# Optimization experiments

Hardware: AMD Instinct MI355X
Metric: run time of the kernel (lower is better)

The kernel has to match this reference:

```python
import jax, jax.numpy as jnp
import numpy as np

N = 512      # num_neurons
D = 32       # delay_dim
T = 8192     # number of sequential timesteps
OMEGA = 10.0 # base_freq
ALPHA = 0.5
DT = 1e-3    # dt_global per tick
TWO_PI = float(2.0 * np.pi)


def setup_inputs() -> dict:
    key = jax.random.key(0)
    k = jax.random.split(key, 6)
    X_real = jax.random.normal(k[0], (T, D), jnp.float32)
    X_imag = jax.random.normal(k[1], (T, D), jnp.float32)
    target_wave = jax.random.normal(k[2], (T,), jnp.float32)
    # W initialized as torch.polar(rand*0.1, rand*2pi)
    mag = jax.random.uniform(k[3], (N, D), jnp.float32) * 0.1
    ang = jax.random.uniform(k[4], (N, D), jnp.float32) * TWO_PI
    W_real = mag * jnp.cos(ang)
    W_imag = mag * jnp.sin(ang)
    phi0 = jax.random.uniform(k[5], (N,), jnp.float32) * TWO_PI
    beta0 = jnp.linspace(0.005, 0.05, N, dtype=jnp.float32)
    return {"X_real": X_real, "X_imag": X_imag, "target_wave": target_wave,
            "W_real": W_real, "W_imag": W_imag, "phi0": phi0, "beta0": beta0}


def _run(X_real, X_imag, target_wave, W_real, W_imag, phi0, beta0):
    W0 = (W_real + 1j * W_imag).astype(jnp.complex64)   # [N, D]
    X = (X_real + 1j * X_imag).astype(jnp.complex64)    # [T, D]
    lt0 = jnp.zeros((N,), jnp.float32)                  # local_time
    err0 = jnp.float32(0.0)                             # err_smooth

    def step(carry, inp):
        W, phi, beta, lt, err = carry
        x, tgt = inp                                    # x: [D] complex, tgt: scalar
        gamma = jnp.exp(-ALPHA * beta)                  # time dilation Γ  [N]
        dt_local = gamma * DT                           # [N]
        lt = lt + dt_local
        Z = W @ x                                       # X_c @ W.T -> [N] complex
        theta = OMEGA * lt + phi                        # [N]
        gate = jax.nn.relu(jnp.cos(theta - jnp.angle(Z)))
        Y = jnp.abs(Z) * gate                           # [N] real
        out = jnp.sum(Y * jnp.cos(theta))               # Re(sum Y * exp(i theta))
        # thermodynamic error feedback (sequential dependency)
        raw_err = jnp.abs(tgt - out)
        err = 0.99 * err + 0.01 * raw_err
        rel_err = err / (jnp.abs(tgt) + 0.01)
        beta_target = 3.5 * jnp.exp(-5.0 * rel_err)
        tau = jnp.where(beta_target > beta, 0.5 / (gamma + 1e-6), 0.03)
        a_s = 1.0 - jnp.exp(-DT / tau)
        beta_new = jnp.clip(beta + a_s * (beta_target - beta), 0.005, 5.0)
        # Hebbian growth / viscous decay (growth.T and decay.T directly in [N,D])
        growth_t = 0.05 * Y[:, None] * x[None, :]                 # [N, D] complex
        decay_t = (beta_new * Y ** 2)[:, None].astype(jnp.complex64) * W
        W = W + (growth_t - decay_t) * dt_local[:, None].astype(jnp.complex64)
        # phase pull: imag(tgt * exp(-i theta)) = -tgt*sin(theta) for real tgt
        phi = jnp.mod(phi + (2.0 / N) * (-tgt * jnp.sin(theta)) * dt_local, TWO_PI)
        return (W, phi, beta_new, lt, err), (out, beta_new, gamma)

    _, (outs, betas, gammas) = jax.lax.scan(
        step, (W0, phi0, beta0, lt0, err0), (X, target_wave))
    return outs, betas, gammas


def reference(X_real, X_imag, target_wave, W_real, W_imag, phi0, beta0):
    return _run(X_real, X_imag, target_wave, W_real, W_imag, phi0, beta0)
```

## Files before the change

### kernel.cpp

```cpp
#include <hip/hip_runtime.h>

#define NN 512
#define DD 32
#define TT 8192

typedef float v4f __attribute__((ext_vector_type(4)));
typedef float v2f __attribute__((ext_vector_type(2)));
typedef __attribute__((address_space(3))) float lds_f;
typedef __attribute__((address_space(3))) void lds_v;
typedef const __attribute__((address_space(1))) void glb_v;

constexpr float F_OMEGA = 10.0f;
constexpr float F_DT = 1e-3f;
constexpr float F_TWO_PI = 6.28318530717958647692f;
constexpr float F_INV_TWO_PI = 0.15915494309189533577f;

__device__ __forceinline__ void barrier_lgkm() {
    asm volatile("s_waitcnt lgkmcnt(0)\n\ts_barrier" ::: "memory");
}

__device__ __forceinline__ void glds4(const float* g, lds_f* dst) {
    __builtin_amdgcn_global_load_lds((glb_v*)g, (lds_v*)dst, 4, 0, 0);
}

#define DSR128(dst, addr, off) \
    asm volatile("ds_read_b128 %0, %1 offset:" #off : "=v"(dst) : "v"(addr))
#define DSR32(dst, addr, off) \
    asm volatile("ds_read_b32 %0, %1 offset:" #off : "=v"(dst) : "v"(addr))

#define PK_MUL(d, a, b)  \
    asm("v_pk_mul_f32 %0, %1, %2" : "=v"(d) : "v"(a), "v"(b))
#define PK_FMA_ACC(d, a, b)  \
    asm("v_pk_fma_f32 %0, %1, %2, %0" : "+v"(d) : "v"(a), "v"(b))
#define PK_FMA_W(w, m, t)  \
    asm("v_pk_fma_f32 %0, %0, %1, %2" : "+v"(w) : "v"(m), "v"(t))

#define DPP_ADD(x, ctrl, rmask)                                                 \
    {                                                                           \
        int _t = __builtin_amdgcn_update_dpp(0, __float_as_int(x),              \
                                             (ctrl), (rmask), 0xf, true);       \
        (x) += __int_as_float(_t);                                              \
    }

__device__ __forceinline__ float wave_reduce_to_lane63(float x) {
    DPP_ADD(x, 0xB1, 0xf);
    DPP_ADD(x, 0x4E, 0xf);
    DPP_ADD(x, 0x141, 0xf);
    DPP_ADD(x, 0x140, 0xf);
    DPP_ADD(x, 0x142, 0xa);
    DPP_ADD(x, 0x143, 0xc);
    return x;
}

__global__ __launch_bounds__(512, 2) void deerskin(
    const float* __restrict__ Xr, const float* __restrict__ Xi,
    const float* __restrict__ Tg,
    const float* __restrict__ W0r, const float* __restrict__ W0i,
    const float* __restrict__ Phi0, const float* __restrict__ Beta0,
    float* __restrict__ outs, float* __restrict__ betas, float* __restrict__ gammas)
{
    __shared__ __align__(16) float xbuf[3][72];
    __shared__ __align__(16) float sP[16];

    const int n = threadIdx.x;
    const int lane = n & 63;
    const int wid = n >> 6;

    v2f wr2[16], wi2[16];
    {
        const v2f* wr0 = (const v2f*)(W0r + n * DD);
        const v2f* wi0 = (const v2f*)(W0i + n * DD);
#pragma unroll
        for (int k = 0; k < 16; ++k) { wr2[k] = wr0[k]; wi2[k] = wi0[k]; }
    }
    float phi = Phi0[n];
    float beta = Beta0[n];
    float lt = 0.0f;
    float err = 0.0f;

    const float* xsrc = ((lane < 32) ? Xr : Xi) + (lane & 31);

    lds_f* pcur = (lds_f*)&xbuf[0][0];
    lds_f* pnxt = (lds_f*)&xbuf[1][0];
    lds_f* pfut = (lds_f*)&xbuf[2][0];

    if (wid == 0) {
        glds4(xsrc, pcur);
        glds4(xsrc + DD, pnxt);
        if (lane == 0) {
            glds4(Tg, pcur + 64);
            glds4(Tg + 1, pnxt + 64);
        }
        asm volatile("s_waitcnt vmcnt(0)" ::: "memory");
    }
    barrier_lgkm();

    for (int t = 0; t < TT; ++t) {
        if (wid == 0) {
            int tf = t + 2; tf = (tf < TT) ? tf : (TT - 1);
            glds4(xsrc + (size_t)tf * DD, pfut);
            if (lane == 0) glds4(Tg + tf, pfut + 64);
        }

        const float gamma = __expf(-0.5f * beta);
        const float dtl = gamma * F_DT;
        lt += dtl;
        const float theta = fmaf(F_OMEGA, lt, phi);
        float rev = theta * F_INV_TWO_PI;
        rev -= floorf(rev);
        const float s = __builtin_amdgcn_sinf(rev);
        const float c = __builtin_amdgcn_cosf(rev);
        const float a_sA = 1.0f - __expf(-2.0f * F_DT * (gamma + 1e-6f));
        const float a_sB = 1.0f - __expf(-F_DT / 0.03f);

        const unsigned lcur = (unsigned)(unsigned long long)pcur;
        v4f cr[8], ci[8];
        float tgt;
        DSR128(cr[0], lcur, 0);   DSR128(cr[1], lcur, 16);
        DSR128(cr[2], lcur, 32);  DSR128(cr[3], lcur, 48);
        DSR128(cr[4], lcur, 64);  DSR128(cr[5], lcur, 80);
        DSR128(cr[6], lcur, 96);  DSR128(cr[7], lcur, 112);
        DSR128(ci[0], lcur, 128); DSR128(ci[1], lcur, 144);
        DSR128(ci[2], lcur, 160); DSR128(ci[3], lcur, 176);
        DSR128(ci[4], lcur, 192); DSR128(ci[5], lcur, 208);
        DSR128(ci[6], lcur, 224); DSR128(ci[7], lcur, 240);
        DSR32(tgt, lcur, 256);
        asm volatile("s_waitcnt lgkmcnt(0)"
            : "+v"(cr[0]), "+v"(cr[1]), "+v"(cr[2]), "+v"(cr[3]),
              "+v"(cr[4]), "+v"(cr[5]), "+v"(cr[6]), "+v"(cr[7]),
              "+v"(ci[0]), "+v"(ci[1]), "+v"(ci[2]), "+v"(ci[3]),
              "+v"(ci[4]), "+v"(ci[5]), "+v"(ci[6]), "+v"(ci[7]),
              "+v"(tgt) :: "memory");

        v2f xr_[16], xi_[16];
#pragma unroll
        for (int j = 0; j < 8; ++j) {
            xr_[2 * j]     = __builtin_shufflevector(cr[j], cr[j], 0, 1);
            xr_[2 * j + 1] = __builtin_shufflevector(cr[j], cr[j], 2, 3);
            xi_[2 * j]     = __builtin_shufflevector(ci[j], ci[j], 0, 1);
            xi_[2 * j + 1] = __builtin_shufflevector(ci[j], ci[j], 2, 3);
        }

        v2f arr0, arr1, aii0, aii1, ari0, ari1, air0, air1;
        PK_MUL(arr0, wr2[0], xr_[0]); PK_MUL(arr1, wr2[1], xr_[1]);
        PK_MUL(aii0, wi2[0], xi_[0]); PK_MUL(aii1, wi2[1], xi_[1]);
        PK_MUL(ari0, wr2[0], xi_[0]); PK_MUL(ari1, wr2[1], xi_[1]);
        PK_MUL(air0, wi2[0], xr_[0]); PK_MUL(air1, wi2[1], xr_[1]);
#pragma unroll
        for (int k = 2; k < 16; k += 2) {
            PK_FMA_ACC(arr0, wr2[k], xr_[k]); PK_FMA_ACC(arr1, wr2[k + 1], xr_[k + 1]);
            PK_FMA_ACC(aii0, wi2[k], xi_[k]); PK_FMA_ACC(aii1, wi2[k + 1], xi_[k + 1]);
            PK_FMA_ACC(ari0, wr2[k], xi_[k]); PK_FMA_ACC(ari1, wr2[k + 1], xi_[k + 1]);
            PK_FMA_ACC(air0, wi2[k], xr_[k]); PK_FMA_ACC(air1, wi2[k + 1], xr_[k + 1]);
        }
        const float hArr = (arr0.x + arr0.y) + (arr1.x + arr1.y);
        const float hAii = (aii0.x + aii0.y) + (aii1.x + aii1.y);
        const float hAri = (ari0.x + ari0.y) + (ari1.x + ari1.y);
        const float hAir = (air0.x + air0.y) + (air1.x + air1.y);
        const float zr = hArr - hAii;
        const float zi = hAri + hAir;

        const float Y = fmaxf(fmaf(zr, c, zi * s), 0.0f);

        float v = wave_reduce_to_lane63(Y * c);
        if (lane == 63) sP[((t & 1) << 3) + wid] = v;

        const float inv_t = 1.0f / (fabsf(tgt) + 0.01f);
        const float yy = Y * Y;
        const float g = 0.05f * Y * dtl;
        phi += (2.0f / (float)NN) * (-tgt * s) * dtl;
        phi = phi - F_TWO_PI * floorf(phi * F_INV_TWO_PI);

        if (wid == 0) asm volatile("s_waitcnt vmcnt(5)" ::: "memory");
        barrier_lgkm();

        const float4* sp4 = (const float4*)(sP + ((t & 1) << 3));
        const float4 p0 = sp4[0], p1 = sp4[1];
        const float out = ((p0.x + p0.y) + (p0.z + p0.w)) +
                          ((p1.x + p1.y) + (p1.z + p1.w));

        const float raw = fabsf(tgt - out);
        err = 0.99f * err + 0.01f * raw;
        const float rel = err * inv_t;
        const float btg = 3.5f * __expf(-5.0f * rel);
        const float a_s = (btg > beta) ? a_sA : a_sB;
        float bnew = beta + a_s * (btg - beta);
        bnew = fminf(fmaxf(bnew, 0.005f), 5.0f);

        const float k = (bnew * yy) * dtl;
        const float m1 = 1.0f - k;
        const v2f m12 = {m1, m1};
        const v2f g2 = {g, g};
#pragma unroll
        for (int q = 0; q < 16; ++q) {
            v2f t0, t1;
            PK_MUL(t0, g2, xr_[q]); PK_FMA_W(wr2[q], m12, t0);
            PK_MUL(t1, g2, xi_[q]); PK_FMA_W(wi2[q], m12, t1);
        }

        gammas[t * NN + n] = gamma;
        betas[t * NN + n] = bnew;
        if (lane == 63) outs[t] = out;
        beta = bnew;

        lds_f* tmp = pcur; pcur = pnxt; pnxt = pfut; pfut = tmp;
    }
}

extern "C" void kernel_launch(void* const* d_in, const int* in_sizes, int n_in,
                              void* d_out, int out_size, void* d_ws, size_t ws_size,
                              hipStream_t stream) {
    const float* Xr    = (const float*)d_in[0];
    const float* Xi    = (const float*)d_in[1];
    const float* Tg    = (const float*)d_in[2];
    const float* W0r   = (const float*)d_in[3];
    const float* W0i   = (const float*)d_in[4];
    const float* Phi0  = (const float*)d_in[5];
    const float* Beta0 = (const float*)d_in[6];

    float* outs   = (float*)d_out;
    float* betas  = outs + TT;
    float* gammas = betas + (size_t)TT * NN;

    deerskin<<<1, NN, 0, stream>>>(Xr, Xi, Tg, W0r, W0i, Phi0, Beta0,
                                   outs, betas, gammas);
}
```

Before: 9.072 ms.

## Prefetch next-step LDS inputs after barrier and precompute growth terms before sync

```diff
diff --git a/kernel.cpp b/kernel.cpp
--- a/kernel.cpp
+++ b/kernel.cpp
@@ -84,6 +84,9 @@
     lds_f* pnxt = (lds_f*)&xbuf[1][0];
     lds_f* pfut = (lds_f*)&xbuf[2][0];
 
+    v4f cr[8], ci[8];
+    float tgt_nxt;
+
     if (wid == 0) {
         glds4(xsrc, pcur);
         glds4(xsrc + DD, pnxt);
@@ -94,12 +97,41 @@
         asm volatile("s_waitcnt vmcnt(0)" ::: "memory");
     }
     barrier_lgkm();
+    {
+        const unsigned l0 = (unsigned)(unsigned long long)pcur;
+        DSR128(cr[0], l0, 0);   DSR128(cr[1], l0, 16);
+        DSR128(cr[2], l0, 32);  DSR128(cr[3], l0, 48);
+        DSR128(cr[4], l0, 64);  DSR128(cr[5], l0, 80);
+        DSR128(cr[6], l0, 96);  DSR128(cr[7], l0, 112);
+        DSR128(ci[0], l0, 128); DSR128(ci[1], l0, 144);
+        DSR128(ci[2], l0, 160); DSR128(ci[3], l0, 176);
+        DSR128(ci[4], l0, 192); DSR128(ci[5], l0, 208);
+        DSR128(ci[6], l0, 224); DSR128(ci[7], l0, 240);
+        DSR32(tgt_nxt, l0, 256);
+    }
 
     for (int t = 0; t < TT; ++t) {
         if (wid == 0) {
             int tf = t + 2; tf = (tf < TT) ? tf : (TT - 1);
             glds4(xsrc + (size_t)tf * DD, pfut);
             if (lane == 0) glds4(Tg + tf, pfut + 64);
+        }
+
+        asm volatile("s_waitcnt lgkmcnt(0)"
+            : "+v"(cr[0]), "+v"(cr[1]), "+v"(cr[2]), "+v"(cr[3]),
+              "+v"(cr[4]), "+v"(cr[5]), "+v"(cr[6]), "+v"(cr[7]),
+              "+v"(ci[0]), "+v"(ci[1]), "+v"(ci[2]), "+v"(ci[3]),
+              "+v"(ci[4]), "+v"(ci[5]), "+v"(ci[6]), "+v"(ci[7]),
+              "+v"(tgt_nxt) :: "memory");
+        const float tgt = tgt_nxt;
+
+        v2f xr_[16], xi_[16];
+#pragma unroll
+        for (int j = 0; j < 8; ++j) {
+            xr_[2 * j]     = __builtin_shufflevector(cr[j], cr[j], 0, 1);
+            xr_[2 * j + 1] = __builtin_shufflevector(cr[j], cr[j], 2, 3);
+            xi_[2 * j]     = __builtin_shufflevector(ci[j], ci[j], 0, 1);
+            xi_[2 * j + 1] = __builtin_shufflevector(ci[j], ci[j], 2, 3);
         }
 
         const float gamma = __expf(-0.5f * beta);
@@ -113,34 +145,6 @@
         const float a_sA = 1.0f - __expf(-2.0f * F_DT * (gamma + 1e-6f));
         const float a_sB = 1.0f - __expf(-F_DT / 0.03f);
 
-        const unsigned lcur = (unsigned)(unsigned long long)pcur;
-        v4f cr[8], ci[8];
-        float tgt;
-        DSR128(cr[0], lcur, 0);   DSR128(cr[1], lcur, 16);
-        DSR128(cr[2], lcur, 32);  DSR128(cr[3], lcur, 48);
-        DSR128(cr[4], lcur, 64);  DSR128(cr[5], lcur, 80);
-        DSR128(cr[6], lcur, 96);  DSR128(cr[7], lcur, 112);
-        DSR128(ci[0], lcur, 128); DSR128(ci[1], lcur, 144);
-        DSR128(ci[2], lcur, 160); DSR128(ci[3], lcur, 176);
-        DSR128(ci[4], lcur, 192); DSR128(ci[5], lcur, 208);
-        DSR128(ci[6], lcur, 224); DSR128(ci[7], lcur, 240);
-        DSR32(tgt, lcur, 256);
-        asm volatile("s_waitcnt lgkmcnt(0)"
-            : "+v"(cr[0]), "+v"(cr[1]), "+v"(cr[2]), "+v"(cr[3]),
-              "+v"(cr[4]), "+v"(cr[5]), "+v"(cr[6]), "+v"(cr[7]),
-              "+v"(ci[0]), "+v"(ci[1]), "+v"(ci[2]), "+v"(ci[3]),
-              "+v"(ci[4]), "+v"(ci[5]), "+v"(ci[6]), "+v"(ci[7]),
-              "+v"(tgt) :: "memory");
-
-        v2f xr_[16], xi_[16];
-#pragma unroll
-        for (int j = 0; j < 8; ++j) {
-            xr_[2 * j]     = __builtin_shufflevector(cr[j], cr[j], 0, 1);
-            xr_[2 * j + 1] = __builtin_shufflevector(cr[j], cr[j], 2, 3);
-            xi_[2 * j]     = __builtin_shufflevector(ci[j], ci[j], 0, 1);
-            xi_[2 * j + 1] = __builtin_shufflevector(ci[j], ci[j], 2, 3);
-        }
-
         v2f arr0, arr1, aii0, aii1, ari0, ari1, air0, air1;
         PK_MUL(arr0, wr2[0], xr_[0]); PK_MUL(arr1, wr2[1], xr_[1]);
         PK_MUL(aii0, wi2[0], xi_[0]); PK_MUL(aii1, wi2[1], xi_[1]);
@@ -168,17 +172,38 @@
         const float inv_t = 1.0f / (fabsf(tgt) + 0.01f);
         const float yy = Y * Y;
         const float g = 0.05f * Y * dtl;
+        const v2f g2 = {g, g};
+        v2f twr[16], twi[16];
+#pragma unroll
+        for (int q = 0; q < 16; ++q) {
+            PK_MUL(twr[q], g2, xr_[q]);
+            PK_MUL(twi[q], g2, xi_[q]);
+        }
         phi += (2.0f / (float)NN) * (-tgt * s) * dtl;
         phi = phi - F_TWO_PI * floorf(phi * F_INV_TWO_PI);
 
         if (wid == 0) asm volatile("s_waitcnt vmcnt(5)" ::: "memory");
         barrier_lgkm();
 
-        const float4* sp4 = (const float4*)(sP + ((t & 1) << 3));
-        const float4 p0 = sp4[0], p1 = sp4[1];
+        const unsigned lsp =
+            (unsigned)(unsigned long long)(lds_f*)&sP[(t & 1) << 3];
+        const unsigned lnx = (unsigned)(unsigned long long)pnxt;
+        v4f p0, p1;
+        DSR128(p0, lsp, 0); DSR128(p1, lsp, 16);
+        DSR128(cr[0], lnx, 0);   DSR128(cr[1], lnx, 16);
+        DSR128(cr[2], lnx, 32);  DSR128(cr[3], lnx, 48);
+        DSR128(cr[4], lnx, 64);  DSR128(cr[5], lnx, 80);
+        DSR128(cr[6], lnx, 96);  DSR128(cr[7], lnx, 112);
+        DSR128(ci[0], lnx, 128); DSR128(ci[1], lnx, 144);
+        DSR128(ci[2], lnx, 160); DSR128(ci[3], lnx, 176);
+        DSR128(ci[4], lnx, 192); DSR128(ci[5], lnx, 208);
+        DSR128(ci[6], lnx, 224);
+        asm volatile("s_waitcnt lgkmcnt(15)" : "+v"(p0), "+v"(p1) :: "memory");
+        DSR128(ci[7], lnx, 240);
+        DSR32(tgt_nxt, lnx, 256);
+
         const float out = ((p0.x + p0.y) + (p0.z + p0.w)) +
                           ((p1.x + p1.y) + (p1.z + p1.w));
-
         const float raw = fabsf(tgt - out);
         err = 0.99f * err + 0.01f * raw;
         const float rel = err * inv_t;
@@ -190,12 +215,10 @@
         const float k = (bnew * yy) * dtl;
         const float m1 = 1.0f - k;
         const v2f m12 = {m1, m1};
-        const v2f g2 = {g, g};
 #pragma unroll
         for (int q = 0; q < 16; ++q) {
-            v2f t0, t1;
-            PK_MUL(t0, g2, xr_[q]); PK_FMA_W(wr2[q], m12, t0);
-            PK_MUL(t1, g2, xi_[q]); PK_FMA_W(wi2[q], m12, t1);
+            PK_FMA_W(wr2[q], m12, twr[q]);
+            PK_FMA_W(wi2[q], m12, twi[q]);
         }
 
         gammas[t * NN + n] = gamma;
```

After: 8.874 ms. -2.2%, faster.

## Load per-step inputs via scalar loads into SGPRs instead of LDS staging

Applied to the files above, without the earlier changes.

```diff
diff --git a/kernel.cpp b/kernel.cpp
--- a/kernel.cpp
+++ b/kernel.cpp
@@ -6,9 +6,8 @@
 
 typedef float v4f __attribute__((ext_vector_type(4)));
 typedef float v2f __attribute__((ext_vector_type(2)));
+typedef float v16f __attribute__((ext_vector_type(16)));
 typedef __attribute__((address_space(3))) float lds_f;
-typedef __attribute__((address_space(3))) void lds_v;
-typedef const __attribute__((address_space(1))) void glb_v;
 
 constexpr float F_OMEGA = 10.0f;
 constexpr float F_DT = 1e-3f;
@@ -19,19 +18,18 @@
     asm volatile("s_waitcnt lgkmcnt(0)\n\ts_barrier" ::: "memory");
 }
 
-__device__ __forceinline__ void glds4(const float* g, lds_f* dst) {
-    __builtin_amdgcn_global_load_lds((glb_v*)g, (lds_v*)dst, 4, 0, 0);
-}
-
 #define DSR128(dst, addr, off) \
     asm volatile("ds_read_b128 %0, %1 offset:" #off : "=v"(dst) : "v"(addr))
-#define DSR32(dst, addr, off) \
-    asm volatile("ds_read_b32 %0, %1 offset:" #off : "=v"(dst) : "v"(addr))
-
-#define PK_MUL(d, a, b)  \
-    asm("v_pk_mul_f32 %0, %1, %2" : "=v"(d) : "v"(a), "v"(b))
-#define PK_FMA_ACC(d, a, b)  \
-    asm("v_pk_fma_f32 %0, %1, %2, %0" : "+v"(d) : "v"(a), "v"(b))
+
+#define SL16(dst, ptr, off) \
+    asm volatile("s_load_dwordx16 %0, %1, " #off : "=s"(dst) : "s"(ptr))
+#define SL1(dst, ptr) \
+    asm volatile("s_load_dword %0, %1, 0x0" : "=s"(dst) : "s"(ptr))
+
+#define PK_MUL_VS(d, a, b)  \
+    asm("v_pk_mul_f32 %0, %1, %2" : "=v"(d) : "v"(a), "s"(b))
+#define PK_FMA_ACC_VS(d, a, b)  \
+    asm("v_pk_fma_f32 %0, %1, %2, %0" : "+v"(d) : "v"(a), "s"(b))
 #define PK_FMA_W(w, m, t)  \
     asm("v_pk_fma_f32 %0, %0, %1, %2" : "+v"(w) : "v"(m), "v"(t))
 
@@ -52,6 +50,24 @@
     return x;
 }
 
+#define MKP(dst, lo, hi)                                                        \
+    dst[0]  = __builtin_shufflevector(lo, lo, 0, 1);                            \
+    dst[1]  = __builtin_shufflevector(lo, lo, 2, 3);                            \
+    dst[2]  = __builtin_shufflevector(lo, lo, 4, 5);                            \
+    dst[3]  = __builtin_shufflevector(lo, lo, 6, 7);                            \
+    dst[4]  = __builtin_shufflevector(lo, lo, 8, 9);                            \
+    dst[5]  = __builtin_shufflevector(lo, lo, 10, 11);                          \
+    dst[6]  = __builtin_shufflevector(lo, lo, 12, 13);                          \
+    dst[7]  = __builtin_shufflevector(lo, lo, 14, 15);                          \
+    dst[8]  = __builtin_shufflevector(hi, hi, 0, 1);                            \
+    dst[9]  = __builtin_shufflevector(hi, hi, 2, 3);                            \
+    dst[10] = __builtin_shufflevector(hi, hi, 4, 5);                            \
+    dst[11] = __builtin_shufflevector(hi, hi, 6, 7);                            \
+    dst[12] = __builtin_shufflevector(hi, hi, 8, 9);                            \
+    dst[13] = __builtin_shufflevector(hi, hi, 10, 11);                          \
+    dst[14] = __builtin_shufflevector(hi, hi, 12, 13);                          \
+    dst[15] = __builtin_shufflevector(hi, hi, 14, 15);
+
 __global__ __launch_bounds__(512, 2) void deerskin(
     const float* __restrict__ Xr, const float* __restrict__ Xi,
     const float* __restrict__ Tg,
@@ -59,7 +75,6 @@
     const float* __restrict__ Phi0, const float* __restrict__ Beta0,
     float* __restrict__ outs, float* __restrict__ betas, float* __restrict__ gammas)
 {
-    __shared__ __align__(16) float xbuf[3][72];
     __shared__ __align__(16) float sP[16];
 
     const int n = threadIdx.x;
@@ -78,30 +93,14 @@
     float lt = 0.0f;
     float err = 0.0f;
 
-    const float* xsrc = ((lane < 32) ? Xr : Xi) + (lane & 31);
-
-    lds_f* pcur = (lds_f*)&xbuf[0][0];
-    lds_f* pnxt = (lds_f*)&xbuf[1][0];
-    lds_f* pfut = (lds_f*)&xbuf[2][0];
-
-    if (wid == 0) {
-        glds4(xsrc, pcur);
-        glds4(xsrc + DD, pnxt);
-        if (lane == 0) {
-            glds4(Tg, pcur + 64);
-            glds4(Tg + 1, pnxt + 64);
-        }
-        asm volatile("s_waitcnt vmcnt(0)" ::: "memory");
-    }
-    barrier_lgkm();
+    v16f sxr0, sxr1, sxi0, sxi1;
+    float stgt;
+
+    SL16(sxr0, Xr, 0x0); SL16(sxr1, Xr, 0x40);
+    SL16(sxi0, Xi, 0x0); SL16(sxi1, Xi, 0x40);
+    SL1(stgt, Tg);
 
     for (int t = 0; t < TT; ++t) {
-        if (wid == 0) {
-            int tf = t + 2; tf = (tf < TT) ? tf : (TT - 1);
-            glds4(xsrc + (size_t)tf * DD, pfut);
-            if (lane == 0) glds4(Tg + tf, pfut + 64);
-        }
-
         const float gamma = __expf(-0.5f * beta);
         const float dtl = gamma * F_DT;
         lt += dtl;
@@ -113,45 +112,26 @@
         const float a_sA = 1.0f - __expf(-2.0f * F_DT * (gamma + 1e-6f));
         const float a_sB = 1.0f - __expf(-F_DT / 0.03f);
 
-        const unsigned lcur = (unsigned)(unsigned long long)pcur;
-        v4f cr[8], ci[8];
-        float tgt;
-        DSR128(cr[0], lcur, 0);   DSR128(cr[1], lcur, 16);
-        DSR128(cr[2], lcur, 32);  DSR128(cr[3], lcur, 48);
-        DSR128(cr[4], lcur, 64);  DSR128(cr[5], lcur, 80);
-        DSR128(cr[6], lcur, 96);  DSR128(cr[7], lcur, 112);
-        DSR128(ci[0], lcur, 128); DSR128(ci[1], lcur, 144);
-        DSR128(ci[2], lcur, 160); DSR128(ci[3], lcur, 176);
-        DSR128(ci[4], lcur, 192); DSR128(ci[5], lcur, 208);
-        DSR128(ci[6], lcur, 224); DSR128(ci[7], lcur, 240);
-        DSR32(tgt, lcur, 256);
         asm volatile("s_waitcnt lgkmcnt(0)"
-            : "+v"(cr[0]), "+v"(cr[1]), "+v"(cr[2]), "+v"(cr[3]),
-              "+v"(cr[4]), "+v"(cr[5]), "+v"(cr[6]), "+v"(cr[7]),
-              "+v"(ci[0]), "+v"(ci[1]), "+v"(ci[2]), "+v"(ci[3]),
-              "+v"(ci[4]), "+v"(ci[5]), "+v"(ci[6]), "+v"(ci[7]),
-              "+v"(tgt) :: "memory");
+            : "+s"(sxr0), "+s"(sxr1), "+s"(sxi0), "+s"(sxi1), "+s"(stgt)
+            :: "memory");
+        const float tgt = stgt;
 
         v2f xr_[16], xi_[16];
-#pragma unroll
-        for (int j = 0; j < 8; ++j) {
-            xr_[2 * j]     = __builtin_shufflevector(cr[j], cr[j], 0, 1);
-            xr_[2 * j + 1] = __builtin_shufflevector(cr[j], cr[j], 2, 3);
-            xi_[2 * j]     = __builtin_shufflevector(ci[j], ci[j], 0, 1);
-            xi_[2 * j + 1] = __builtin_shufflevector(ci[j], ci[j], 2, 3);
-        }
+        MKP(xr_, sxr0, sxr1);
+        MKP(xi_, sxi0, sxi1);
 
         v2f arr0, arr1, aii0, aii1, ari0, ari1, air0, air1;
-        PK_MUL(arr0, wr2[0], xr_[0]); PK_MUL(arr1, wr2[1], xr_[1]);
-        PK_MUL(aii0, wi2[0], xi_[0]); PK_MUL(aii1, wi2[1], xi_[1]);
-        PK_MUL(ari0, wr2[0], xi_[0]); PK_MUL(ari1, wr2[1], xi_[1]);
-        PK_MUL(air0, wi2[0], xr_[0]); PK_MUL(air1, wi2[1], xr_[1]);
+        PK_MUL_VS(arr0, wr2[0], xr_[0]); PK_MUL_VS(arr1, wr2[1], xr_[1]);
+        PK_MUL_VS(aii0, wi2[0], xi_[0]); PK_MUL_VS(aii1, wi2[1], xi_[1]);
+        PK_MUL_VS(ari0, wr2[0], xi_[0]); PK_MUL_VS(ari1, wr2[1], xi_[1]);
+        PK_MUL_VS(air0, wi2[0], xr_[0]); PK_MUL_VS(air1, wi2[1], xr_[1]);
 #pragma unroll
         for (int k = 2; k < 16; k += 2) {
-            PK_FMA_ACC(arr0, wr2[k], xr_[k]); PK_FMA_ACC(arr1, wr2[k + 1], xr_[k + 1]);
-            PK_FMA_ACC(aii0, wi2[k], xi_[k]); PK_FMA_ACC(aii1, wi2[k + 1], xi_[k + 1]);
-            PK_FMA_ACC(ari0, wr2[k], xi_[k]); PK_FMA_ACC(ari1, wr2[k + 1], xi_[k + 1]);
-            PK_FMA_ACC(air0, wi2[k], xr_[k]); PK_FMA_ACC(air1, wi2[k + 1], xr_[k + 1]);
+            PK_FMA_ACC_VS(arr0, wr2[k], xr_[k]); PK_FMA_ACC_VS(arr1, wr2[k + 1], xr_[k + 1]);
+            PK_FMA_ACC_VS(aii0, wi2[k], xi_[k]); PK_FMA_ACC_VS(aii1, wi2[k + 1], xi_[k + 1]);
+            PK_FMA_ACC_VS(ari0, wr2[k], xi_[k]); PK_FMA_ACC_VS(ari1, wr2[k + 1], xi_[k + 1]);
+            PK_FMA_ACC_VS(air0, wi2[k], xr_[k]); PK_FMA_ACC_VS(air1, wi2[k + 1], xr_[k + 1]);
         }
         const float hArr = (arr0.x + arr0.y) + (arr1.x + arr1.y);
         const float hAii = (aii0.x + aii0.y) + (aii1.x + aii1.y);
@@ -168,17 +148,37 @@
         const float inv_t = 1.0f / (fabsf(tgt) + 0.01f);
         const float yy = Y * Y;
         const float g = 0.05f * Y * dtl;
+        const v2f g2 = {g, g};
+        v2f twr[16], twi[16];
+#pragma unroll
+        for (int q = 0; q < 16; ++q) {
+            PK_MUL_VS(twr[q], g2, xr_[q]);
+            PK_MUL_VS(twi[q], g2, xi_[q]);
+        }
         phi += (2.0f / (float)NN) * (-tgt * s) * dtl;
         phi = phi - F_TWO_PI * floorf(phi * F_INV_TWO_PI);
-
-        if (wid == 0) asm volatile("s_waitcnt vmcnt(5)" ::: "memory");
+        gammas[t * NN + n] = gamma;
+
         barrier_lgkm();
 
-        const float4* sp4 = (const float4*)(sP + ((t & 1) << 3));
-        const float4 p0 = sp4[0], p1 = sp4[1];
+        const unsigned lsp =
+            (unsigned)(unsigned long long)(lds_f*)&sP[(t & 1) << 3];
+        v4f p0, p1;
+        DSR128(p0, lsp, 0); DSR128(p1, lsp, 16);
+        asm volatile("s_waitcnt lgkmcnt(0)" : "+v"(p0), "+v"(p1) :: "memory");
+
+        {
+            const int tn = (t + 1 < TT) ? (t + 1) : (TT - 1);
+            const float* xrp = Xr + (size_t)tn * DD;
+            const float* xip = Xi + (size_t)tn * DD;
+            const float* tgp = Tg + tn;
+            SL16(sxr0, xrp, 0x0); SL16(sxr1, xrp, 0x40);
+            SL16(sxi0, xip, 0x0); SL16(sxi1, xip, 0x40);
+            SL1(stgt, tgp);
+        }
+
         const float out = ((p0.x + p0.y) + (p0.z + p0.w)) +
                           ((p1.x + p1.y) + (p1.z + p1.w));
-
         const float raw = fabsf(tgt - out);
         err = 0.99f * err + 0.01f * raw;
         const float rel = err * inv_t;
@@ -190,20 +190,15 @@
         const float k = (bnew * yy) * dtl;
         const float m1 = 1.0f - k;
         const v2f m12 = {m1, m1};
-        const v2f g2 = {g, g};
 #pragma unroll
         for (int q = 0; q < 16; ++q) {
-            v2f t0, t1;
-            PK_MUL(t0, g2, xr_[q]); PK_FMA_W(wr2[q], m12, t0);
-            PK_MUL(t1, g2, xi_[q]); PK_FMA_W(wi2[q], m12, t1);
-        }
-
-        gammas[t * NN + n] = gamma;
+            PK_FMA_W(wr2[q], m12, twr[q]);
+            PK_FMA_W(wi2[q], m12, twi[q]);
+        }
+
         betas[t * NN + n] = bnew;
         if (lane == 63) outs[t] = out;
         beta = bnew;
-
-        lds_f* tmp = pcur; pcur = pnxt; pnxt = pfut; pfut = tmp;
     }
 }
 
```

Measured after the change: 8.506 ms. 1.07x faster.
